# Optimization experiments

Measured on AMD Instinct MI355X. Metric: run time of the kernel, lower is better.

## Reference

```python
import jax, jax.numpy as jnp
import numpy as np

D = 128      # hidden_dim
NH = 4       # nhead
FF = 64      # dim_feedforward
P = 16       # patch size
C, H, W = 3, 224, 224
NA = 15      # n_actions
BS = 256
NP = (H // P) * (W // P)      # 196 patches
PD = C * P * P                # 768 patch_dim


def _ln(x, s, b):
    m = jnp.mean(x, -1, keepdims=True)
    v = jnp.mean(jnp.square(x - m), -1, keepdims=True)
    return (x - m) / jnp.sqrt(v + 1e-5) * s + b


def _mha(q, k, v, Wqkv, bqkv, Wo, bo):
    # q,k,v: (L, B, D); Wqkv: (D, 3D) jax-layout; torch MultiheadAttention math
    Wq, Wk, Wv = jnp.split(Wqkv, 3, axis=1)
    bq, bk, bv = jnp.split(bqkv, 3)
    hd = D // NH
    Lq, B, _ = q.shape
    Lk = k.shape[0]
    Q = (q @ Wq + bq).reshape(Lq, B, NH, hd)
    K = (k @ Wk + bk).reshape(Lk, B, NH, hd)
    V = (v @ Wv + bv).reshape(Lk, B, NH, hd)
    scores = jnp.einsum('qbhd,kbhd->bhqk', Q, K) * np.float32(1.0 / np.sqrt(hd))
    attn = jax.nn.softmax(scores, axis=-1)
    out = jnp.einsum('bhqk,kbhd->qbhd', attn, V).reshape(Lq, B, D)
    return out @ Wo + bo


def setup_inputs() -> dict:
    key = jax.random.key(0)
    ks = iter(jax.random.split(key, 64))
    n = lambda shape, sc=0.02: (jax.random.normal(next(ks), shape, jnp.float32) * sc)
    inp = {
        'image': jax.random.normal(next(ks), (BS, C, H, W), jnp.float32),
        'angle': jax.random.normal(next(ks), (BS,), jnp.float32),
        'pos_x': jax.random.normal(next(ks), (BS,), jnp.float32),
        'pos_y': jax.random.normal(next(ks), (BS,), jnp.float32),
        'sk': jax.random.normal(next(ks), (BS, 200), jnp.float32),
        'patch_W': n((PD, D)), 'patch_b': n((D,)),
        'pos_emb': n((NP, 1, D), 1.0),
        'enc_qkv_W': n((D, 3 * D)), 'enc_qkv_b': n((3 * D,)),
        'enc_out_W': n((D, D)), 'enc_out_b': n((D,)),
        'enc_ln1_s': jnp.ones((D,)), 'enc_ln1_b': jnp.zeros((D,)),
        'enc_ff1_W': n((D, FF)), 'enc_ff1_b': n((FF,)),
        'enc_ff2_W': n((FF, D)), 'enc_ff2_b': n((D,)),
        'enc_ln2_s': jnp.ones((D,)), 'enc_ln2_b': jnp.zeros((D,)),
        'dec_sa_qkv_W': n((D, 3 * D)), 'dec_sa_qkv_b': n((3 * D,)),
        'dec_sa_out_W': n((D, D)), 'dec_sa_out_b': n((D,)),
        'dec_ca_qkv_W': n((D, 3 * D)), 'dec_ca_qkv_b': n((3 * D,)),
        'dec_ca_out_W': n((D, D)), 'dec_ca_out_b': n((D,)),
        'dec_ln1_s': jnp.ones((D,)), 'dec_ln1_b': jnp.zeros((D,)),
        'dec_ln2_s': jnp.ones((D,)), 'dec_ln2_b': jnp.zeros((D,)),
        'dec_ln3_s': jnp.ones((D,)), 'dec_ln3_b': jnp.zeros((D,)),
        'dec_ff1_W': n((D, FF)), 'dec_ff1_b': n((FF,)),
        'dec_ff2_W': n((FF, D)), 'dec_ff2_b': n((D,)),
        'dec_norm_s': jnp.ones((D,)), 'dec_norm_b': jnp.zeros((D,)),
        'sk1_W': n((200, 256)), 'sk1_b': n((256,)),
        'sk2_W': n((256, 256)), 'sk2_b': n((256,)),
        'sk3_W': n((256, 100)), 'sk3_b': n((100,)),
        'act_W': n((NA + 103, D)), 'act_b': n((D,)),
        'l1_W': n((D, D)), 'l1_b': n((D,)),
        'l2_W': n((D, 1)), 'l2_b': n((1,)),
    }
    return inp


def reference(image, angle, pos_x, pos_y, sk,
              patch_W, patch_b, pos_emb,
              enc_qkv_W, enc_qkv_b, enc_out_W, enc_out_b,
              enc_ln1_s, enc_ln1_b, enc_ff1_W, enc_ff1_b, enc_ff2_W, enc_ff2_b,
              enc_ln2_s, enc_ln2_b,
              dec_sa_qkv_W, dec_sa_qkv_b, dec_sa_out_W, dec_sa_out_b,
              dec_ca_qkv_W, dec_ca_qkv_b, dec_ca_out_W, dec_ca_out_b,
              dec_ln1_s, dec_ln1_b, dec_ln2_s, dec_ln2_b, dec_ln3_s, dec_ln3_b,
              dec_ff1_W, dec_ff1_b, dec_ff2_W, dec_ff2_b,
              dec_norm_s, dec_norm_b,
              sk1_W, sk1_b, sk2_W, sk2_b, sk3_W, sk3_b,
              act_W, act_b, l1_W, l1_b, l2_W, l2_b):
    b = image.shape[0]
    hh, ww = H // P, W // P
    # rearrange 'b c (h p1) (w p2) -> b (h w) (p1 p2 c)'
    x = image.reshape(b, C, hh, P, ww, P).transpose(0, 2, 4, 3, 5, 1).reshape(b, hh * ww, PD)
    src = (x @ patch_W + patch_b).transpose(1, 0, 2) + pos_emb  # (n, b, D)
    # encoder layer (post-norm, dropout=eval)
    s2 = _mha(src, src, src, enc_qkv_W, enc_qkv_b, enc_out_W, enc_out_b)
    src = _ln(src + s2, enc_ln1_s, enc_ln1_b)
    ff = jax.nn.relu(src @ enc_ff1_W + enc_ff1_b) @ enc_ff2_W + enc_ff2_b
    memory = _ln(src + ff, enc_ln2_s, enc_ln2_b)
    # sketch MLP
    s = jax.nn.relu(sk @ sk1_W + sk1_b)
    s = jax.nn.relu(s @ sk2_W + sk2_b)
    s = s @ sk3_W + sk3_b  # (b, 100)
    pos_ang = jnp.stack([angle, pos_x, pos_y], axis=1)  # (b, 3)
    # batched action encoding (replaces python double loop)
    nA = NA
    eye = jnp.broadcast_to(jnp.eye(nA, dtype=image.dtype)[None], (b, nA, nA))
    feats = jnp.concatenate([
        eye,
        jnp.broadcast_to(pos_ang[:, None, :], (b, nA, 3)),
        jnp.broadcast_to(s[:, None, :], (b, nA, 100)),
    ], axis=-1)  # (b, nA, nA+103)
    tgt = (feats @ act_W + act_b).transpose(1, 0, 2)  # (nA, b, D)
    # decoder layer (post-norm)
    t2 = _mha(tgt, tgt, tgt, dec_sa_qkv_W, dec_sa_qkv_b, dec_sa_out_W, dec_sa_out_b)
    tgt = _ln(tgt + t2, dec_ln1_s, dec_ln1_b)
    t2 = _mha(tgt, memory, memory, dec_ca_qkv_W, dec_ca_qkv_b, dec_ca_out_W, dec_ca_out_b)
    tgt = _ln(tgt + t2, dec_ln2_s, dec_ln2_b)
    ff = jax.nn.relu(tgt @ dec_ff1_W + dec_ff1_b) @ dec_ff2_W + dec_ff2_b
    tgt = _ln(tgt + ff, dec_ln3_s, dec_ln3_b)
    out = _ln(tgt, dec_norm_s, dec_norm_b)  # (nA, b, D)
    out = out.transpose(1, 0, 2)  # (b, nA, D)
    q = jax.nn.relu(out @ l1_W + l1_b) @ l2_W + l2_b  # (b, nA, 1)
    return q[..., 0]  # (b, nA)
```

## Files before the change

### kernel.cpp

```cpp
#include <hip/hip_runtime.h>
#include <math.h>

#define BSZ 256
#define DIM 128
#define NHD 4
#define NPATCH 196
#define NACT 15

typedef float f32x4 __attribute__((ext_vector_type(4)));
typedef __bf16 bf16x8 __attribute__((ext_vector_type(8)));
typedef short short8 __attribute__((ext_vector_type(8)));

__device__ __forceinline__ float wred_sum(float v) {
#pragma unroll
    for (int m = 1; m < 64; m <<= 1) v += __shfl_xor(v, m, 64);
    return v;
}
__device__ __forceinline__ float wred_max(float v) {
#pragma unroll
    for (int m = 1; m < 64; m <<= 1) v = fmaxf(v, __shfl_xor(v, m, 64));
    return v;
}
__device__ __forceinline__ ushort f2bf(float f) {
    unsigned u = __float_as_uint(f);
    return (ushort)((u + 0x7fffu + ((u >> 16) & 1u)) >> 16);
}

__global__ __launch_bounds__(256) void k_wconv(
    const float* __restrict__ pW, const float* __restrict__ qkvW,
    const float* __restrict__ outW, const float* __restrict__ ff1W,
    const float* __restrict__ ff2W, const float* __restrict__ ckvW,
    ushort* __restrict__ o)
{
    int i = blockIdx.x * 256 + threadIdx.x;
    if (i < 98304) {
        int n = i / 768, kp = i % 768;
        int c = kp >> 8, q = kp & 255;
        o[i] = f2bf(pW[(q * 3 + c) * 128 + n]); return;
    }
    i -= 98304;
    if (i < 49152) { int n = i >> 7, k = i & 127; o[98304 + i] = f2bf(qkvW[k * 384 + n]); return; }
    i -= 49152;
    if (i < 16384) { int n = i >> 7, k = i & 127; o[147456 + i] = f2bf(outW[k * 128 + n]); return; }
    i -= 16384;
    if (i < 8192)  { int n = i >> 7, k = i & 127; o[163840 + i] = f2bf(ff1W[k * 64 + n]); return; }
    i -= 8192;
    if (i < 8192)  { int n = i >> 6, k = i & 63;  o[172032 + i] = f2bf(ff2W[k * 128 + n]); return; }
    i -= 8192;
    if (i < 32768) { int n = i >> 7, k = i & 127; o[180224 + i] = f2bf(ckvW[k * 384 + 128 + n]); return; }
}

__global__ __launch_bounds__(512) void k_pg_dec1(
    const float* __restrict__ img, const ushort* __restrict__ Wt,
    const float* __restrict__ pbias, const float* __restrict__ pe,
    float* __restrict__ C,
    const ushort* __restrict__ qkvWt, const float* __restrict__ qkvB,
    ushort* __restrict__ QKVb,
    const float* __restrict__ sk,
    const float* __restrict__ W1, const float* __restrict__ b1,
    const float* __restrict__ W2, const float* __restrict__ b2,
    const float* __restrict__ W3, const float* __restrict__ b3,
    const float* __restrict__ ang, const float* __restrict__ px,
    const float* __restrict__ py,
    const float* __restrict__ actW, const float* __restrict__ actb,
    const float* __restrict__ saW, const float* __restrict__ sab,
    const float* __restrict__ saoW, const float* __restrict__ saob,
    const float* __restrict__ ln1s, const float* __restrict__ ln1b,
    const float* __restrict__ caW, const float* __restrict__ cab,
    float* __restrict__ TGo, float* __restrict__ DQ)
{
    extern __shared__ char smem[];
    const int t = threadIdx.x;
    const int w = t >> 6, l = t & 63;

    if (blockIdx.x >= 256) {
        ushort* As = (ushort*)smem;
        ushort* Ws = As + 2 * 64 * 64;
        const bool act = t < 256;
        const int pb = blockIdx.x - 256;
        const int p = pb >> 2, bq = pb & 3;
        const int hp_ = p / 14, wp = p % 14;
        const int r0 = p * 256 + bq * 64;
        const int wm = w >> 1, wn = w & 1;
        const int lrow = l & 15, lk = l >> 4;
        const int arow = (t & 255) >> 2;
        const int b_img = bq * 64 + arow;
        const float* gimg = img + (size_t)b_img * 150528 + hp_ * 3584 + wp * 16;

        f32x4 acc[2][4];
#pragma unroll
        for (int m = 0; m < 2; ++m)
#pragma unroll
            for (int n = 0; n < 4; ++n) acc[m][n] = (f32x4)0.f;

        float4 va[4];
        short8 wr[4];

        auto loadT = [&](int kc) {
            if (!act) return;
            const int c = kc >> 8, p1q = (kc >> 6) & 3;
            const float* gc = gimg + c * 50176 + p1q * 896;
#pragma unroll
            for (int i = 0; i < 4; ++i)
                va[i] = *(const float4*)(gc + i * 224 + (t & 3) * 4);
#pragma unroll
            for (int j = 0; j < 4; ++j) {
                const int i2 = t + 256 * j;
                const int row = i2 >> 3, ch = i2 & 7;
                wr[j] = *(const short8*)(Wt + (size_t)row * 768 + kc + ch * 8);
            }
        };
        auto storeT = [&](int buf) {
            if (!act) return;
            ushort* Ab = As + buf * 64 * 64;
            ushort* Wb = Ws + buf * 128 * 64;
#pragma unroll
            for (int i = 0; i < 4; ++i) {
                ushort4 o4;
                o4.x = f2bf(va[i].x); o4.y = f2bf(va[i].y);
                o4.z = f2bf(va[i].z); o4.w = f2bf(va[i].w);
                const int kq = (t & 3) + 4 * i;
                const int bo = (kq * 8) ^ ((arow & 7) << 4);
                *(ushort4*)((char*)Ab + arow * 128 + bo) = o4;
            }
#pragma unroll
            for (int j = 0; j < 4; ++j) {
                const int i2 = t + 256 * j;
                const int row = i2 >> 3, ch = i2 & 7;
                const int sw = (ch * 16) ^ ((row & 7) << 4);
                *(short8*)((char*)Wb + row * 128 + sw) = wr[j];
            }
        };
        auto mfmaT = [&](int buf) {
            if (!act) return;
            const ushort* Ab = As + buf * 64 * 64;
            const ushort* Wb = Ws + buf * 128 * 64;
#pragma unroll
            for (int ks = 0; ks < 2; ++ks) {
                bf16x8 af[2], bfr[4];
#pragma unroll
                for (int m = 0; m < 2; ++m) {
                    const int row = wm * 32 + m * 16 + lrow;
                    const int col = (ks * 64 + lk * 16) ^ ((row & 7) << 4);
                    af[m] = *(const bf16x8*)((const char*)Ab + row * 128 + col);
                }
#pragma unroll
                for (int n = 0; n < 4; ++n) {
                    const int row = wn * 64 + n * 16 + lrow;
                    const int col = (ks * 64 + lk * 16) ^ ((row & 7) << 4);
                    bfr[n] = *(const bf16x8*)((const char*)Wb + row * 128 + col);
                }
#pragma unroll
                for (int m = 0; m < 2; ++m)
#pragma unroll
                    for (int n = 0; n < 4; ++n)
                        acc[m][n] = __builtin_amdgcn_mfma_f32_16x16x32_bf16(
                            af[m], bfr[n], acc[m][n], 0, 0, 0);
            }
        };

        loadT(0);
        for (int it = 0; it < 12; it += 2) {
            storeT(0);
            if (it + 1 < 12) loadT((it + 1) * 64);
            __syncthreads();
            mfmaT(0);
            storeT(1);
            if (it + 2 < 12) loadT((it + 2) * 64);
            __syncthreads();
            mfmaT(1);
        }

        __syncthreads();
        const int crow0 = (l >> 4) * 4;
        const int ccol = l & 15;
        if (act) {
#pragma unroll
            for (int m = 0; m < 2; ++m) {
                const int rowb = wm * 32 + m * 16 + crow0;
#pragma unroll
                for (int n = 0; n < 4; ++n) {
                    const int col = wn * 64 + n * 16 + ccol;
                    const float bv = pbias[col] + pe[p * 128 + col];
#pragma unroll
                    for (int j = 0; j < 4; ++j) {
                        const int row = rowb + j;
                        const float v = acc[m][n][j] + bv;
                        C[(size_t)(r0 + row) * 128 + col] = v;
                        const int bo = row * 256 + (((col >> 3) * 16) ^ ((row & 7) << 4)) + (col & 7) * 2;
                        *(ushort*)((char*)As + bo) = f2bf(v);
                    }
                }
            }
        }

        const int wm2 = w >> 1;
        const int wn2 = w & 1;
        for (int cc = 0; cc < 3; ++cc) {
            __syncthreads();
            for (int i = t; i < 2048; i += 512) {
                const int row = i >> 4, ch = i & 15;
                *(short8*)((char*)Ws + row * 256 + ((ch * 16) ^ ((row & 7) << 4))) =
                    *(const short8*)(qkvWt + (size_t)(cc * 128 + row) * 128 + ch * 8);
            }
            __syncthreads();
            f32x4 a2[4];
#pragma unroll
            for (int n = 0; n < 4; ++n) a2[n] = (f32x4)0.f;
#pragma unroll
            for (int ks = 0; ks < 4; ++ks) {
                const int arow2 = wm2 * 16 + lrow;
                const int acol = (ks * 64 + lk * 16) ^ ((arow2 & 7) << 4);
                const bf16x8 af = *(const bf16x8*)((const char*)As + arow2 * 256 + acol);
#pragma unroll
                for (int n = 0; n < 4; ++n) {
                    const int brow = wn2 * 64 + n * 16 + lrow;
                    const int bcol = (ks * 64 + lk * 16) ^ ((brow & 7) << 4);
                    const bf16x8 bf = *(const bf16x8*)((const char*)Ws + brow * 256 + bcol);
                    a2[n] = __builtin_amdgcn_mfma_f32_16x16x32_bf16(af, bf, a2[n], 0, 0, 0);
                }
            }
#pragma unroll
            for (int n = 0; n < 4; ++n) {
                const int gcol = cc * 128 + wn2 * 64 + n * 16 + ccol;
                const float bb = qkvB[gcol];
#pragma unroll
                for (int j = 0; j < 4; ++j) {
                    const int grow = r0 + wm2 * 16 + crow0 + j;
                    QKVb[(size_t)grow * 384 + gcol] = f2bf(a2[n][j] + bb);
                }
            }
        }
        return;
    }

    float* tg  = (float*)smem;
    float* qkv = tg + 1920;
    float* ao  = qkv + 5820;
    float* xr  = ao + 1920;
    float* h1  = xr + 256;
    float* h2  = h1 + 256;
    float* s3  = h2 + 256;
    float* pbv = s3 + 100;
    float* hp  = pbv + 64;
    const int b = blockIdx.x;

    {
        float pf = 0.f;
#define PFW(P, N) for (int i = t * 32; i < (N); i += 512 * 32) pf += P[i];
        PFW(W1, 200 * 256)
        PFW(W2, 256 * 256)
        PFW(W3, 256 * 100)
        PFW(actW, 118 * 128)
        PFW(saW, 128 * 384)
        PFW(saoW, 128 * 128)
        PFW(caW, 128 * 384)
#undef PFW
        asm volatile("" :: "v"(pf));
    }

    if (t < 256) xr[t] = (t < 200) ? sk[(size_t)b * 200 + t] : 0.f;
    __syncthreads();
    {
        const int c = t & 255, g = t >> 8;
        const int k0 = g * 100;
        float a = 0.f;
#pragma unroll 10
        for (int k = k0; k < k0 + 100; ++k) a += xr[k] * W1[k * 256 + c];
        hp[g * 256 + c] = a;
    }
    __syncthreads();
    if (t < 256) h1[t] = fmaxf(hp[t] + hp[256 + t] + b1[t], 0.f);
    __syncthreads();
    {
        const int c = t & 255, g = t >> 8;
        const int k0 = g * 128;
        float a = 0.f;
#pragma unroll 8
        for (int k = k0; k < k0 + 128; ++k) a += h1[k] * W2[k * 256 + c];
        hp[g * 256 + c] = a;
    }
    __syncthreads();
    if (t < 256) h2[t] = fmaxf(hp[t] + hp[256 + t] + b2[t], 0.f);
    __syncthreads();
    if (t < 400) {
        const int c = t % 100, g = t / 100;
        const int k0 = g * 64;
        float a = 0.f;
#pragma unroll 8
        for (int k = k0; k < k0 + 64; ++k) a += h2[k] * W3[k * 100 + c];
        hp[g * 256 + c] = a;
    }
    __syncthreads();
    if (t < 100) s3[t] = hp[t] + hp[256 + t] + hp[512 + t] + hp[768 + t] + b3[t];
    __syncthreads();
    {
        const int c = t & 127, g = t >> 7;
        const int k0 = g * 25;
        float a = 0.f;
#pragma unroll 5
        for (int k = k0; k < k0 + 25; ++k) a += s3[k] * actW[(18 + k) * 128 + c];
        hp[g * 256 + c] = a;
    }
    __syncthreads();
    if (t < 128) {
        const float base = actb[t] + hp[t] + hp[256 + t] + hp[512 + t] + hp[768 + t] +
                           ang[b] * actW[15 * 128 + t] + px[b] * actW[16 * 128 + t] +
                           py[b] * actW[17 * 128 + t];
#pragma unroll
        for (int i = 0; i < 15; ++i) tg[i * 128 + t] = base + actW[i * 128 + t];
    }
    __syncthreads();

    if (t < 384) {
        float acc[15];
#pragma unroll
        for (int r = 0; r < 15; ++r) acc[r] = 0.f;
#pragma unroll 4
        for (int k = 0; k < 128; ++k) {
            const float wv = saW[(size_t)k * 384 + t];
#pragma unroll
            for (int r = 0; r < 15; ++r) acc[r] += tg[r * 128 + k] * wv;
        }
        const float bb = sab[t];
#pragma unroll
        for (int r = 0; r < 15; ++r) qkv[r * 388 + t] = acc[r] + bb;
    }
    __syncthreads();

    const float rs = 0.17677669529663687f;
    if (w < 4) {
        for (int qi = 0; qi < 15; ++qi) {
            float s = -3.0e38f;
            if (l < 15) {
                s = 0.f;
#pragma unroll
                for (int d = 0; d < 32; ++d)
                    s += qkv[qi * 388 + w * 32 + d] * qkv[l * 388 + 128 + w * 32 + d];
                s *= rs;
            }
            const float m = wred_max(s);
            const float pv = (l < 15) ? __expf(s - m) : 0.f;
            const float sum = wred_sum(pv);
            if (l < 15) pbv[w * 16 + l] = pv;
            if (l < 32) {
                float o = 0.f;
#pragma unroll
                for (int j = 0; j < 15; ++j) o += pbv[w * 16 + j] * qkv[j * 388 + 256 + w * 32 + l];
                ao[qi * 128 + w * 32 + l] = o / sum;
            }
        }
    }
    __syncthreads();

    {
        const int c = t & 127, g = t >> 7;
        const int r3 = (g + 12 < 15) ? g + 12 : 0;
        float a0 = 0.f, a1 = 0.f, a2 = 0.f, a3 = 0.f;
#pragma unroll 4
        for (int k = 0; k < 128; ++k) {
            const float wv = saoW[(size_t)k * 128 + c];
            a0 += ao[g * 128 + k] * wv;
            a1 += ao[(g + 4) * 128 + k] * wv;
            a2 += ao[(g + 8) * 128 + k] * wv;
            a3 += ao[r3 * 128 + k] * wv;
        }
        const float bb = saob[c];
        qkv[g * 388 + c]       = a0 + bb + tg[g * 128 + c];
        qkv[(g + 4) * 388 + c] = a1 + bb + tg[(g + 4) * 128 + c];
        qkv[(g + 8) * 388 + c] = a2 + bb + tg[(g + 8) * 128 + c];
        if (g + 12 < 15) qkv[(g + 12) * 388 + c] = a3 + bb + tg[(g + 12) * 128 + c];
    }
    __syncthreads();
    for (int r = w; r < 15; r += 8) {
        const float x0 = qkv[r * 388 + l], x1 = qkv[r * 388 + l + 64];
        const float sm = wred_sum(x0 + x1);
        const float sq = wred_sum(x0 * x0 + x1 * x1);
        const float mean = sm * 0.0078125f;
        const float rstd = rsqrtf(sq * 0.0078125f - mean * mean + 1e-5f);
        const float y0 = (x0 - mean) * rstd * ln1s[l] + ln1b[l];
        const float y1 = (x1 - mean) * rstd * ln1s[l + 64] + ln1b[l + 64];
        tg[r * 128 + l] = y0; tg[r * 128 + l + 64] = y1;
        float* g2 = TGo + ((size_t)r * 256 + b) * 128;
        g2[l] = y0; g2[l + 64] = y1;
    }
    __syncthreads();

    {
        const int c = t & 127, g = t >> 7;
        const int r3 = (g + 12 < 15) ? g + 12 : 0;
        float a0 = 0.f, a1 = 0.f, a2 = 0.f, a3 = 0.f;
#pragma unroll 4
        for (int k = 0; k < 128; ++k) {
            const float wv = caW[(size_t)k * 384 + c];
            a0 += tg[g * 128 + k] * wv;
            a1 += tg[(g + 4) * 128 + k] * wv;
            a2 += tg[(g + 8) * 128 + k] * wv;
            a3 += tg[r3 * 128 + k] * wv;
        }
        const float bb = cab[c];
        DQ[((size_t)g * 256 + b) * 128 + c]       = a0 + bb;
        DQ[((size_t)(g + 4) * 256 + b) * 128 + c] = a1 + bb;
        DQ[((size_t)(g + 8) * 256 + b) * 128 + c] = a2 + bb;
        if (g + 12 < 15) DQ[((size_t)(g + 12) * 256 + b) * 128 + c] = a3 + bb;
    }
}

template <int FF, int CKV>
__global__ __launch_bounds__(256) void k_gemm_ln(
    const ushort* __restrict__ A, int lda,
    const ushort* __restrict__ Wt, int K,
    const float* __restrict__ bias,
    const float* __restrict__ resid,
    const float* __restrict__ lns, const float* __restrict__ lnbi,
    float* __restrict__ Co, ushort* __restrict__ Cb,
    const ushort* __restrict__ ffW, const float* __restrict__ ffb,
    ushort* __restrict__ Fb,
    const ushort* __restrict__ ckvW, const float* __restrict__ ckvB,
    float* __restrict__ KVout)
{
    __shared__ ushort As[64 * 64];
    __shared__ ushort Ws[128 * 64];
    __shared__ float psum[64][2][2];
    __shared__ ushort ffWs[FF ? 64 * 128 : 2];
    __shared__ ushort ckvWs[CKV ? 64 * 128 : 2];
    const int t = threadIdx.x;
    const int w = t >> 6, l = t & 63;
    const int r0 = blockIdx.x * 64;
    const int wm = w >> 1, wn = w & 1;
    const int lrow = l & 15, lk = l >> 4;

    f32x4 acc[2][4];
#pragma unroll
    for (int m = 0; m < 2; ++m)
#pragma unroll
        for (int n = 0; n < 4; ++n) acc[m][n] = (f32x4)0.f;

    for (int kc = 0; kc < K; kc += 64) {
        __syncthreads();
#pragma unroll
        for (int i = t; i < 64 * 8; i += 256) {
            const int row = i >> 3, ch = i & 7;
            const int sw = (ch * 16) ^ ((row & 7) << 4);
            *(short8*)((char*)As + row * 128 + sw) =
                *(const short8*)(A + (size_t)(r0 + row) * lda + kc + ch * 8);
        }
#pragma unroll
        for (int i = t; i < 128 * 8; i += 256) {
            const int row = i >> 3, ch = i & 7;
            const int sw = (ch * 16) ^ ((row & 7) << 4);
            *(short8*)((char*)Ws + row * 128 + sw) =
                *(const short8*)(Wt + (size_t)row * K + kc + ch * 8);
        }
        __syncthreads();
#pragma unroll
        for (int ks = 0; ks < 2; ++ks) {
            bf16x8 af[2], bfr[4];
#pragma unroll
            for (int m = 0; m < 2; ++m) {
                const int row = wm * 32 + m * 16 + lrow;
                const int col = (ks * 64 + lk * 16) ^ ((row & 7) << 4);
                af[m] = *(const bf16x8*)((const char*)As + row * 128 + col);
            }
#pragma unroll
            for (int n = 0; n < 4; ++n) {
                const int row = wn * 64 + n * 16 + lrow;
                const int col = (ks * 64 + lk * 16) ^ ((row & 7) << 4);
                bfr[n] = *(const bf16x8*)((const char*)Ws + row * 128 + col);
            }
#pragma unroll
            for (int m = 0; m < 2; ++m)
#pragma unroll
                for (int n = 0; n < 4; ++n)
                    acc[m][n] = __builtin_amdgcn_mfma_f32_16x16x32_bf16(
                        af[m], bfr[n], acc[m][n], 0, 0, 0);
        }
    }

    const int crow0 = (l >> 4) * 4;
    const int ccol = l & 15;
#pragma unroll
    for (int m = 0; m < 2; ++m) {
        const int growb = r0 + wm * 32 + m * 16 + crow0;
#pragma unroll
        for (int n = 0; n < 4; ++n) {
            const int gcol = wn * 64 + n * 16 + ccol;
            const float bv = bias[gcol];
#pragma unroll
            for (int j = 0; j < 4; ++j) {
                float v = acc[m][n][j] + bv;
                if (resid) v += resid[(size_t)(growb + j) * 128 + gcol];
                acc[m][n][j] = v;
            }
        }
    }
#pragma unroll
    for (int m = 0; m < 2; ++m)
#pragma unroll
        for (int j = 0; j < 4; ++j) {
            float s_ = 0.f, q_ = 0.f;
#pragma unroll
            for (int n = 0; n < 4; ++n) {
                const float x = acc[m][n][j];
                s_ += x; q_ += x * x;
            }
#pragma unroll
            for (int mk = 1; mk < 16; mk <<= 1) {
                s_ += __shfl_xor(s_, mk, 64);
                q_ += __shfl_xor(q_, mk, 64);
            }
            if (ccol == 0) {
                const int r = wm * 32 + m * 16 + crow0 + j;
                psum[r][wn][0] = s_;
                psum[r][wn][1] = q_;
            }
        }
    __syncthreads();
    float mean_[2][4], rstd_[2][4];
#pragma unroll
    for (int m = 0; m < 2; ++m)
#pragma unroll
        for (int j = 0; j < 4; ++j) {
            const int r = wm * 32 + m * 16 + crow0 + j;
            const float sum = psum[r][0][0] + psum[r][1][0];
            const float sq  = psum[r][0][1] + psum[r][1][1];
            const float mean = sum * 0.0078125f;
            const float var = sq * 0.0078125f - mean * mean;
            mean_[m][j] = mean;
            rstd_[m][j] = rsqrtf(var + 1e-5f);
        }
#pragma unroll
    for (int m = 0; m < 2; ++m) {
        const int growb = r0 + wm * 32 + m * 16 + crow0;
#pragma unroll
        for (int n = 0; n < 4; ++n) {
            const int gcol = wn * 64 + n * 16 + ccol;
            const float sv = lns[gcol], bv2 = lnbi[gcol];
#pragma unroll
            for (int j = 0; j < 4; ++j) {
                const float y = (acc[m][n][j] - mean_[m][j]) * rstd_[m][j] * sv + bv2;
                acc[m][n][j] = y;
                const size_t oi = (size_t)(growb + j) * 128 + gcol;
                if (Co) Co[oi] = y;
                if (Cb) Cb[oi] = f2bf(y);
            }
        }
    }

    if constexpr (FF || CKV) {
#pragma unroll
        for (int m = 0; m < 2; ++m) {
            const int rowb = wm * 32 + m * 16 + crow0;
#pragma unroll
            for (int n = 0; n < 4; ++n) {
                const int c = wn * 64 + n * 16 + ccol;
                const int cb = ((c >> 3) * 16);
#pragma unroll
                for (int j = 0; j < 4; ++j) {
                    const int row = rowb + j;
                    const int bo = row * 256 + ((cb) ^ ((row & 7) << 4)) + (c & 7) * 2;
                    *(ushort*)((char*)Ws + bo) = f2bf(acc[m][n][j]);
                }
            }
        }
    }

    if constexpr (FF) {
        for (int i = t; i < 1024; i += 256) {
            const int row = i >> 4, ch = i & 15;
            *(short8*)((char*)ffWs + row * 256 + ((ch * 16) ^ ((row & 7) << 4))) =
                *(const short8*)(ffW + (size_t)row * 128 + ch * 8);
        }
        __syncthreads();
        f32x4 accF[4];
#pragma unroll
        for (int n = 0; n < 4; ++n) accF[n] = (f32x4)0.f;
#pragma unroll
        for (int ks = 0; ks < 4; ++ks) {
            const int arow2 = w * 16 + lrow;
            const int acol = (ks * 64 + lk * 16) ^ ((arow2 & 7) << 4);
            const bf16x8 af = *(const bf16x8*)((const char*)Ws + arow2 * 256 + acol);
#pragma unroll
            for (int n = 0; n < 4; ++n) {
                const int brow = n * 16 + lrow;
                const int bcol = (ks * 64 + lk * 16) ^ ((brow & 7) << 4);
                const bf16x8 bf = *(const bf16x8*)((const char*)ffWs + brow * 256 + bcol);
                accF[n] = __builtin_amdgcn_mfma_f32_16x16x32_bf16(af, bf, accF[n], 0, 0, 0);
            }
        }
#pragma unroll
        for (int n = 0; n < 4; ++n) {
            const int gcol = n * 16 + ccol;
            const float bb = ffb[gcol];
#pragma unroll
            for (int j = 0; j < 4; ++j) {
                const int grow = r0 + w * 16 + crow0 + j;
                Fb[(size_t)grow * 64 + gcol] = f2bf(fmaxf(accF[n][j] + bb, 0.f));
            }
        }
    }

    if constexpr (CKV) {
        for (int cc = 0; cc < 4; ++cc) {
            __syncthreads();
            for (int i = t; i < 1024; i += 256) {
                const int row = i >> 4, ch = i & 15;
                *(short8*)((char*)ckvWs + row * 256 + ((ch * 16) ^ ((row & 7) << 4))) =
                    *(const short8*)(ckvW + (size_t)(cc * 64 + row) * 128 + ch * 8);
            }
            __syncthreads();
            f32x4 accC[4];
#pragma unroll
            for (int n = 0; n < 4; ++n) accC[n] = (f32x4)0.f;
#pragma unroll
            for (int ks = 0; ks < 4; ++ks) {
                const int arow2 = w * 16 + lrow;
                const int acol = (ks * 64 + lk * 16) ^ ((arow2 & 7) << 4);
                const bf16x8 af = *(const bf16x8*)((const char*)Ws + arow2 * 256 + acol);
#pragma unroll
                for (int n = 0; n < 4; ++n) {
                    const int brow = n * 16 + lrow;
                    const int bcol = (ks * 64 + lk * 16) ^ ((brow & 7) << 4);
                    const bf16x8 bf = *(const bf16x8*)((const char*)ckvWs + brow * 256 + bcol);
                    accC[n] = __builtin_amdgcn_mfma_f32_16x16x32_bf16(af, bf, accC[n], 0, 0, 0);
                }
            }
#pragma unroll
            for (int n = 0; n < 4; ++n) {
                const int gcol = cc * 64 + n * 16 + ccol;
                const float bb = ckvB[gcol];
#pragma unroll
                for (int j = 0; j < 4; ++j) {
                    const int grow = r0 + w * 16 + crow0 + j;
                    KVout[(size_t)grow * 256 + gcol] = accC[n][j] + bb;
                }
            }
        }
    }
}

__global__ __launch_bounds__(256) void k_attn_mfma(
    const ushort* __restrict__ qkv, ushort* __restrict__ ob, float scale)
{
    __shared__ ushort Ks[208 * 40];
    __shared__ ushort Vt[32 * 232];
    __shared__ ushort Ps[4][16 * 232];
    const int bh = blockIdx.x;
    const int b = bh >> 2, h = bh & 3;
    const int t = threadIdx.x, w = t >> 6, l = t & 63;
    const int lr = l & 15, lg = l >> 4;

    for (int idx = t; idx < 784; idx += 256) {
        const int j = idx >> 2, ch = idx & 3;
        const size_t base = ((size_t)j * 256 + b) * 384 + h * 32 + ch * 8;
        *(short8*)(Ks + j * 40 + ch * 8) = *(const short8*)(qkv + base + 128);
        short8 v = *(const short8*)(qkv + base + 256);
#pragma unroll
        for (int q = 0; q < 8; ++q)
            Vt[(ch * 8 + q) * 232 + j] = (ushort)v[q];
    }
    for (int idx = t; idx < 32 * 36; idx += 256)
        Vt[(idx / 36) * 232 + 196 + (idx % 36)] = 0;
    for (int i = l; i < 256; i += 64)
        Ps[w][(i >> 4) * 232 + 208 + (i & 15)] = 0;
    __syncthreads();

    for (int qt = w; qt < 13; qt += 4) {
        int qr = qt * 16 + lr; if (qr > 195) qr = 195;
        const bf16x8 qf = *(const bf16x8*)(qkv + ((size_t)qr * 256 + b) * 384 + h * 32 + lg * 8);

        f32x4 s[13];
#pragma unroll
        for (int jn = 0; jn < 13; ++jn) {
            const bf16x8 kf = *(const bf16x8*)(Ks + (jn * 16 + lr) * 40 + lg * 8);
            s[jn] = __builtin_amdgcn_mfma_f32_16x16x32_bf16(qf, kf, (f32x4)0.f, 0, 0, 0);
        }
        if (lr >= 4) {
            s[12][0] = -3.0e38f; s[12][1] = -3.0e38f;
            s[12][2] = -3.0e38f; s[12][3] = -3.0e38f;
        }

        float inv[4];
        ushort* pw = Ps[w];
#pragma unroll
        for (int j = 0; j < 4; ++j) {
            float m = s[0][j];
#pragma unroll
            for (int jn = 1; jn < 13; ++jn) m = fmaxf(m, s[jn][j]);
            m = fmaxf(m, __shfl_xor(m, 1, 64));
            m = fmaxf(m, __shfl_xor(m, 2, 64));
            m = fmaxf(m, __shfl_xor(m, 4, 64));
            m = fmaxf(m, __shfl_xor(m, 8, 64));
            float sum = 0.f;
#pragma unroll
            for (int jn = 0; jn < 13; ++jn) {
                const float p = __expf((s[jn][j] - m) * scale);
                s[jn][j] = p;
                sum += p;
            }
            sum += __shfl_xor(sum, 1, 64);
            sum += __shfl_xor(sum, 2, 64);
            sum += __shfl_xor(sum, 4, 64);
            sum += __shfl_xor(sum, 8, 64);
            inv[j] = 1.0f / sum;
        }
#pragma unroll
        for (int jn = 0; jn < 13; ++jn)
#pragma unroll
            for (int j = 0; j < 4; ++j)
                pw[(lg * 4 + j) * 232 + jn * 16 + lr] = f2bf(s[jn][j]);

        f32x4 o0 = (f32x4)0.f, o1 = (f32x4)0.f;
#pragma unroll
        for (int kt = 0; kt < 7; ++kt) {
            const bf16x8 pf = *(const bf16x8*)(pw + lr * 232 + kt * 32 + lg * 8);
            const bf16x8 v0 = *(const bf16x8*)(Vt + lr * 232 + kt * 32 + lg * 8);
            const bf16x8 v1 = *(const bf16x8*)(Vt + (16 + lr) * 232 + kt * 32 + lg * 8);
            o0 = __builtin_amdgcn_mfma_f32_16x16x32_bf16(pf, v0, o0, 0, 0, 0);
            o1 = __builtin_amdgcn_mfma_f32_16x16x32_bf16(pf, v1, o1, 0, 0, 0);
        }
#pragma unroll
        for (int j = 0; j < 4; ++j) {
            const int r = qt * 16 + lg * 4 + j;
            if (r < 196) {
                const size_t o = ((size_t)r * 256 + b) * 128 + h * 32;
                ob[o + lr]      = f2bf(o0[j] * inv[j]);
                ob[o + 16 + lr] = f2bf(o1[j] * inv[j]);
            }
        }
    }
}

__global__ __launch_bounds__(256) void k_attn(
    const float* __restrict__ qp, int qstride,
    const float* __restrict__ kvp, int kvstride, int koff, int voff,
    float* __restrict__ op, ushort* __restrict__ ob,
    int Lq, int Lk, float scale)
{
    __shared__ float Kl[196 * 36];
    __shared__ float Vl[196 * 32];
    __shared__ float pbuf[4][256];
    const int bh = blockIdx.x;
    const int b = bh >> 2;
    const int h = bh & 3;
    const int t = threadIdx.x;
    const int w = t >> 6;
    const int l = t & 63;

    for (int idx = t; idx < Lk * 8; idx += 256) {
        const int j = idx >> 3;
        const int kq = idx & 7;
        const size_t row = ((size_t)j * 256 + b) * kvstride + h * 32 + kq * 4;
        *(float4*)(&Kl[j * 36 + kq * 4]) = *(const float4*)(kvp + row + koff);
        *(float4*)(&Vl[j * 32 + kq * 4]) = *(const float4*)(kvp + row + voff);
    }
    if ((Lk & 1) && t < 8) *(float4*)(&Vl[Lk * 32 + t * 4]) = make_float4(0.f, 0.f, 0.f, 0.f);
    __syncthreads();

    const int Lh = (Lk + 1) >> 1;
    const int half = l >> 5;
    const int kk = l & 31;
    const int jb = half * Lh;

    for (int jq = w; jq < Lq; jq += 4) {
        const float* qrow = qp + ((size_t)jq * 256 + b) * qstride + h * 32;
        float4 q4[8];
#pragma unroll
        for (int kq = 0; kq < 8; ++kq) q4[kq] = *(const float4*)(qrow + kq * 4);

        float s[4];
#pragma unroll
        for (int r = 0; r < 4; ++r) {
            const int j = l + (r << 6);
            float acc = -3.0e38f;
            if (j < Lk) {
                acc = 0.f;
#pragma unroll
                for (int kq = 0; kq < 8; ++kq) {
                    const float4 kv = *(const float4*)(&Kl[j * 36 + kq * 4]);
                    acc += q4[kq].x * kv.x + q4[kq].y * kv.y +
                           q4[kq].z * kv.z + q4[kq].w * kv.w;
                }
                acc *= scale;
            }
            s[r] = acc;
        }
        float m = fmaxf(fmaxf(s[0], s[1]), fmaxf(s[2], s[3]));
        m = wred_max(m);
        float sum = 0.f;
#pragma unroll
        for (int r = 0; r < 4; ++r) {
            const int j = l + (r << 6);
            float p = __expf(s[r] - m);
            if (j >= Lk) p = 0.f;
            pbuf[w][j] = p;
            sum += p;
        }
        sum = wred_sum(sum);
        const float inv = 1.0f / sum;
        __threadfence_block();

        float o = 0.f;
        for (int jj = 0; jj < Lh; ++jj) {
            const float pv = pbuf[w][jb + jj];
            const float vv = Vl[(jb + jj) * 32 + kk];
            o += pv * vv;
        }
        o += __shfl_xor(o, 32, 64);
        o *= inv;
        if (l < 32) {
            const size_t oi = ((size_t)jq * 256 + b) * 128 + h * 32 + l;
            if (op) op[oi] = o;
            if (ob) ob[oi] = f2bf(o);
        }
        __threadfence_block();
    }
}

__global__ __launch_bounds__(512) void k_dec2(
    const float* __restrict__ TGo, const float* __restrict__ AT,
    const float* __restrict__ caoW, const float* __restrict__ caob,
    const float* __restrict__ ln2s, const float* __restrict__ ln2b,
    const float* __restrict__ ff1W, const float* __restrict__ ff1b,
    const float* __restrict__ ff2W, const float* __restrict__ ff2b,
    const float* __restrict__ ln3s, const float* __restrict__ ln3b,
    const float* __restrict__ ns, const float* __restrict__ nb,
    const float* __restrict__ l1W, const float* __restrict__ l1b,
    const float* __restrict__ l2w, const float* __restrict__ l2b,
    float* __restrict__ qout)
{
    __shared__ float tg[15][128], ao[15][128], o2[15][128];
    __shared__ float ff[15][64];
    const int b = blockIdx.x, t = threadIdx.x;
    const int w = t >> 6, l = t & 63;

    {
        float pf = 0.f;
#define PFW(P, N) for (int i = t * 32; i < (N); i += 512 * 32) pf += P[i];
        PFW(caoW, 128 * 128)
        PFW(ff1W, 128 * 64)
        PFW(ff2W, 64 * 128)
        PFW(l1W, 128 * 128)
#undef PFW
        asm volatile("" :: "v"(pf));
    }

    for (int idx = t; idx < 1920; idx += 512) {
        const int r = idx >> 7, c = idx & 127;
        tg[r][c] = TGo[((size_t)r * 256 + b) * 128 + c];
        ao[r][c] = AT[((size_t)r * 256 + b) * 128 + c];
    }
    __syncthreads();

    {
        const int c = t & 127, g = t >> 7;
        const int r3 = (g + 12 < 15) ? g + 12 : 0;
        float a0 = 0.f, a1 = 0.f, a2 = 0.f, a3 = 0.f;
#pragma unroll 4
        for (int k = 0; k < 128; ++k) {
            const float wv = caoW[(size_t)k * 128 + c];
            a0 += ao[g][k] * wv;
            a1 += ao[g + 4][k] * wv;
            a2 += ao[g + 8][k] * wv;
            a3 += ao[r3][k] * wv;
        }
        const float bb = caob[c];
        o2[g][c]     = a0 + bb + tg[g][c];
        o2[g + 4][c] = a1 + bb + tg[g + 4][c];
        o2[g + 8][c] = a2 + bb + tg[g + 8][c];
        if (g + 12 < 15) o2[g + 12][c] = a3 + bb + tg[g + 12][c];
    }
    __syncthreads();
    for (int r = w; r < 15; r += 8) {
        const float x0 = o2[r][l], x1 = o2[r][l + 64];
        const float sm = wred_sum(x0 + x1);
        const float sq = wred_sum(x0 * x0 + x1 * x1);
        const float mean = sm * 0.0078125f;
        const float rstd = rsqrtf(sq * 0.0078125f - mean * mean + 1e-5f);
        tg[r][l]      = (x0 - mean) * rstd * ln2s[l] + ln2b[l];
        tg[r][l + 64] = (x1 - mean) * rstd * ln2s[l + 64] + ln2b[l + 64];
    }
    __syncthreads();
    {
        const int n = t & 63, g = t >> 6;
        const int r1 = (g + 8 < 15) ? g + 8 : 0;
        float a0 = 0.f, a1 = 0.f;
#pragma unroll 4
        for (int k = 0; k < 128; ++k) {
            const float wv = ff1W[(size_t)k * 64 + n];
            a0 += tg[g][k] * wv;
            a1 += tg[r1][k] * wv;
        }
        const float bb = ff1b[n];
        ff[g][n] = fmaxf(a0 + bb, 0.f);
        if (g + 8 < 15) ff[g + 8][n] = fmaxf(a1 + bb, 0.f);
    }
    __syncthreads();
    {
        const int c = t & 127, g = t >> 7;
        const int r3 = (g + 12 < 15) ? g + 12 : 0;
        float a0 = 0.f, a1 = 0.f, a2 = 0.f, a3 = 0.f;
#pragma unroll 4
        for (int k = 0; k < 64; ++k) {
            const float wv = ff2W[(size_t)k * 128 + c];
            a0 += ff[g][k] * wv;
            a1 += ff[g + 4][k] * wv;
            a2 += ff[g + 8][k] * wv;
            a3 += ff[r3][k] * wv;
        }
        const float bb = ff2b[c];
        o2[g][c]     = a0 + bb + tg[g][c];
        o2[g + 4][c] = a1 + bb + tg[g + 4][c];
        o2[g + 8][c] = a2 + bb + tg[g + 8][c];
        if (g + 12 < 15) o2[g + 12][c] = a3 + bb + tg[g + 12][c];
    }
    __syncthreads();
    for (int r = w; r < 15; r += 8) {
        const float x0 = o2[r][l], x1 = o2[r][l + 64];
        const float sm = wred_sum(x0 + x1);
        const float sq = wred_sum(x0 * x0 + x1 * x1);
        const float mean = sm * 0.0078125f;
        const float rstd = rsqrtf(sq * 0.0078125f - mean * mean + 1e-5f);
        const float y0 = (x0 - mean) * rstd * ln3s[l] + ln3b[l];
        const float y1 = (x1 - mean) * rstd * ln3s[l + 64] + ln3b[l + 64];
        const float sm2 = wred_sum(y0 + y1);
        const float sq2 = wred_sum(y0 * y0 + y1 * y1);
        const float mean2 = sm2 * 0.0078125f;
        const float rstd2 = rsqrtf(sq2 * 0.0078125f - mean2 * mean2 + 1e-5f);
        tg[r][l]      = (y0 - mean2) * rstd2 * ns[l] + nb[l];
        tg[r][l + 64] = (y1 - mean2) * rstd2 * ns[l + 64] + nb[l + 64];
    }
    __syncthreads();
    {
        const int c = t & 127, g = t >> 7;
        const int r3 = (g + 12 < 15) ? g + 12 : 0;
        float a0 = 0.f, a1 = 0.f, a2 = 0.f, a3 = 0.f;
#pragma unroll 4
        for (int k = 0; k < 128; ++k) {
            const float wv = l1W[(size_t)k * 128 + c];
            a0 += tg[g][k] * wv;
            a1 += tg[g + 4][k] * wv;
            a2 += tg[g + 8][k] * wv;
            a3 += tg[r3][k] * wv;
        }
        const float bb = l1b[c];
        o2[g][c]     = fmaxf(a0 + bb, 0.f);
        o2[g + 4][c] = fmaxf(a1 + bb, 0.f);
        o2[g + 8][c] = fmaxf(a2 + bb, 0.f);
        if (g + 12 < 15) o2[g + 12][c] = fmaxf(a3 + bb, 0.f);
    }
    __syncthreads();
    for (int r = w; r < 15; r += 8) {
        const float d = wred_sum(o2[r][l] * l2w[l] + o2[r][l + 64] * l2w[l + 64]);
        if (l == 0) qout[b * 15 + r] = d + l2b[0];
    }
}

extern "C" void kernel_launch(void* const* d_in, const int* in_sizes, int n_in,
                              void* d_out, int out_size, void* d_ws, size_t ws_size,
                              hipStream_t stream)
{
    (void)in_sizes; (void)n_in; (void)out_size; (void)ws_size;
    const float* image      = (const float*)d_in[0];
    const float* angle      = (const float*)d_in[1];
    const float* pos_x      = (const float*)d_in[2];
    const float* pos_y      = (const float*)d_in[3];
    const float* sk         = (const float*)d_in[4];
    const float* patch_W    = (const float*)d_in[5];
    const float* patch_b    = (const float*)d_in[6];
    const float* pos_emb    = (const float*)d_in[7];
    const float* enc_qkv_W  = (const float*)d_in[8];
    const float* enc_qkv_b  = (const float*)d_in[9];
    const float* enc_out_W  = (const float*)d_in[10];
    const float* enc_out_b  = (const float*)d_in[11];
    const float* enc_ln1_s  = (const float*)d_in[12];
    const float* enc_ln1_b  = (const float*)d_in[13];
    const float* enc_ff1_W  = (const float*)d_in[14];
    const float* enc_ff1_b  = (const float*)d_in[15];
    const float* enc_ff2_W  = (const float*)d_in[16];
    const float* enc_ff2_b  = (const float*)d_in[17];
    const float* enc_ln2_s  = (const float*)d_in[18];
    const float* enc_ln2_b  = (const float*)d_in[19];
    const float* dec_sa_qkv_W = (const float*)d_in[20];
    const float* dec_sa_qkv_b = (const float*)d_in[21];
    const float* dec_sa_out_W = (const float*)d_in[22];
    const float* dec_sa_out_b = (const float*)d_in[23];
    const float* dec_ca_qkv_W = (const float*)d_in[24];
    const float* dec_ca_qkv_b = (const float*)d_in[25];
    const float* dec_ca_out_W = (const float*)d_in[26];
    const float* dec_ca_out_b = (const float*)d_in[27];
    const float* dec_ln1_s  = (const float*)d_in[28];
    const float* dec_ln1_b  = (const float*)d_in[29];
    const float* dec_ln2_s  = (const float*)d_in[30];
    const float* dec_ln2_b  = (const float*)d_in[31];
    const float* dec_ln3_s  = (const float*)d_in[32];
    const float* dec_ln3_b  = (const float*)d_in[33];
    const float* dec_ff1_W  = (const float*)d_in[34];
    const float* dec_ff1_b  = (const float*)d_in[35];
    const float* dec_ff2_W  = (const float*)d_in[36];
    const float* dec_ff2_b  = (const float*)d_in[37];
    const float* dec_norm_s = (const float*)d_in[38];
    const float* dec_norm_b = (const float*)d_in[39];
    const float* sk1_W = (const float*)d_in[40];
    const float* sk1_b = (const float*)d_in[41];
    const float* sk2_W = (const float*)d_in[42];
    const float* sk2_b = (const float*)d_in[43];
    const float* sk3_W = (const float*)d_in[44];
    const float* sk3_b = (const float*)d_in[45];
    const float* act_W = (const float*)d_in[46];
    const float* act_b = (const float*)d_in[47];
    const float* l1_W  = (const float*)d_in[48];
    const float* l1_b  = (const float*)d_in[49];
    const float* l2_W  = (const float*)d_in[50];
    const float* l2_b  = (const float*)d_in[51];

    float* ws = (float*)d_ws;
    float* S0   = ws;
    float* QKVr = ws + 6422528;
    float* T0   = ws + 25690112;
    float* T1   = ws + 32112640;
    float* F1   = ws + 38535168;
    float* M0r  = ws + 41746432;
    float* S1s  = ws + 48168960;
    float* TG   = S1s + 156672;
    ushort* WTS = (ushort*)(ws + 48817152);

    ushort* QKVb = (ushort*)QKVr;
    float*  KV   = QKVr;
    float* DQ   = QKVr + 14319616;
    float* DT0  = T0;
    ushort* T0b  = (ushort*)M0r;
    ushort* F1b  = (ushort*)F1;
    ushort* wt_patch = WTS;
    ushort* wt_qkv   = WTS + 98304;
    ushort* wt_out   = WTS + 147456;
    ushort* wt_ff1   = WTS + 163840;
    ushort* wt_ff2   = WTS + 172032;
    ushort* wt_ckv   = WTS + 180224;
    (void)T1;

    const float rs = 0.17677669529663687f;

    k_wconv<<<dim3(832), 256, 0, stream>>>(patch_W, enc_qkv_W, enc_out_W,
                                           enc_ff1_W, enc_ff2_W, dec_ca_qkv_W, WTS);

    k_pg_dec1<<<dim3(1040), 512, 49152, stream>>>(
        image, wt_patch, patch_b, pos_emb, S0,
        wt_qkv, enc_qkv_b, QKVb,
        sk, sk1_W, sk1_b, sk2_W, sk2_b, sk3_W, sk3_b,
        angle, pos_x, pos_y, act_W, act_b,
        dec_sa_qkv_W, dec_sa_qkv_b, dec_sa_out_W, dec_sa_out_b,
        dec_ln1_s, dec_ln1_b, dec_ca_qkv_W, dec_ca_qkv_b, TG, DQ);

    k_attn_mfma<<<dim3(1024), 256, 0, stream>>>(QKVb, T0b, rs);
    k_gemm_ln<1, 0><<<dim3(784), 256, 0, stream>>>(
        T0b, 128, wt_out, 128, enc_out_b, S0, enc_ln1_s, enc_ln1_b, S0, nullptr,
        wt_ff1, enc_ff1_b, F1b, nullptr, nullptr, nullptr);
    k_gemm_ln<0, 1><<<dim3(784), 256, 0, stream>>>(
        F1b, 64, wt_ff2, 64, enc_ff2_b, S0, enc_ln2_s, enc_ln2_b, nullptr, nullptr,
        nullptr, nullptr, nullptr, wt_ckv, dec_ca_qkv_b + 128, KV);

    k_attn<<<dim3(1024), 256, 0, stream>>>(DQ, 128, KV, 256, 0, 128,
                                           DT0, nullptr, 15, 196, rs);
    k_dec2<<<dim3(256), 512, 0, stream>>>(
        TG, DT0, dec_ca_out_W, dec_ca_out_b, dec_ln2_s, dec_ln2_b,
        dec_ff1_W, dec_ff1_b, dec_ff2_W, dec_ff2_b,
        dec_ln3_s, dec_ln3_b, dec_norm_s, dec_norm_b,
        l1_W, l1_b, l2_W, l2_b, (float*)d_out);
}
```

Baseline: 280.7 us.

## Shrink fused patch/decoder kernel LDS to raise occupancy

The patch-embedding GEMM drops from double-buffered to single-buffered LDS tiles and adds a barrier each k-step. The QKV projection now stages the weight in 64-row chunks over six passes instead of 128-row chunks over three. The decoder branch overlays its scratch buffers onto the qkv region. Together these cut dynamic shared memory from 48KB to 40KB so more blocks can be resident per CU, at the cost of extra synchronisation and less load/compute overlap.

```diff
diff --git a/kernel.cpp b/kernel.cpp
--- a/kernel.cpp
+++ b/kernel.cpp
@@ -75,7 +75,8 @@
 
     if (blockIdx.x >= 256) {
         ushort* As = (ushort*)smem;
-        ushort* Ws = As + 2 * 64 * 64;
+        ushort* WsP = As + 64 * 64;
+        ushort* Wq = As + 8192;
         const bool act = t < 256;
         const int pb = blockIdx.x - 256;
         const int p = pb >> 2, bq = pb & 3;
@@ -110,10 +111,8 @@
                 wr[j] = *(const short8*)(Wt + (size_t)row * 768 + kc + ch * 8);
             }
         };
-        auto storeT = [&](int buf) {
+        auto storeT = [&]() {
             if (!act) return;
-            ushort* Ab = As + buf * 64 * 64;
-            ushort* Wb = Ws + buf * 128 * 64;
 #pragma unroll
             for (int i = 0; i < 4; ++i) {
                 ushort4 o4;
@@ -121,20 +120,18 @@
                 o4.z = f2bf(va[i].z); o4.w = f2bf(va[i].w);
                 const int kq = (t & 3) + 4 * i;
                 const int bo = (kq * 8) ^ ((arow & 7) << 4);
-                *(ushort4*)((char*)Ab + arow * 128 + bo) = o4;
+                *(ushort4*)((char*)As + arow * 128 + bo) = o4;
             }
 #pragma unroll
             for (int j = 0; j < 4; ++j) {
                 const int i2 = t + 256 * j;
                 const int row = i2 >> 3, ch = i2 & 7;
                 const int sw = (ch * 16) ^ ((row & 7) << 4);
-                *(short8*)((char*)Wb + row * 128 + sw) = wr[j];
+                *(short8*)((char*)WsP + row * 128 + sw) = wr[j];
             }
         };
-        auto mfmaT = [&](int buf) {
+        auto mfmaT = [&]() {
             if (!act) return;
-            const ushort* Ab = As + buf * 64 * 64;
-            const ushort* Wb = Ws + buf * 128 * 64;
 #pragma unroll
             for (int ks = 0; ks < 2; ++ks) {
                 bf16x8 af[2], bfr[4];
@@ -142,13 +139,13 @@
                 for (int m = 0; m < 2; ++m) {
                     const int row = wm * 32 + m * 16 + lrow;
                     const int col = (ks * 64 + lk * 16) ^ ((row & 7) << 4);
-                    af[m] = *(const bf16x8*)((const char*)Ab + row * 128 + col);
+                    af[m] = *(const bf16x8*)((const char*)As + row * 128 + col);
                 }
 #pragma unroll
                 for (int n = 0; n < 4; ++n) {
                     const int row = wn * 64 + n * 16 + lrow;
                     const int col = (ks * 64 + lk * 16) ^ ((row & 7) << 4);
-                    bfr[n] = *(const bf16x8*)((const char*)Wb + row * 128 + col);
+                    bfr[n] = *(const bf16x8*)((const char*)WsP + row * 128 + col);
                 }
 #pragma unroll
                 for (int m = 0; m < 2; ++m)
@@ -160,15 +157,12 @@
         };
 
         loadT(0);
-        for (int it = 0; it < 12; it += 2) {
-            storeT(0);
+        for (int it = 0; it < 12; ++it) {
+            __syncthreads();
+            storeT();
             if (it + 1 < 12) loadT((it + 1) * 64);
             __syncthreads();
-            mfmaT(0);
-            storeT(1);
-            if (it + 2 < 12) loadT((it + 2) * 64);
-            __syncthreads();
-            mfmaT(1);
+            mfmaT();
         }
 
         __syncthreads();
@@ -196,33 +190,33 @@
 
         const int wm2 = w >> 1;
         const int wn2 = w & 1;
-        for (int cc = 0; cc < 3; ++cc) {
+        for (int cc = 0; cc < 6; ++cc) {
+            if (cc) __syncthreads();
+            for (int i = t; i < 1024; i += 512) {
+                const int row = i >> 4, ch = i & 15;
+                *(short8*)((char*)Wq + row * 256 + ((ch * 16) ^ ((row & 7) << 4))) =
+                    *(const short8*)(qkvWt + (size_t)(cc * 64 + row) * 128 + ch * 8);
+            }
             __syncthreads();
-            for (int i = t; i < 2048; i += 512) {
-                const int row = i >> 4, ch = i & 15;
-                *(short8*)((char*)Ws + row * 256 + ((ch * 16) ^ ((row & 7) << 4))) =
-                    *(const short8*)(qkvWt + (size_t)(cc * 128 + row) * 128 + ch * 8);
-            }
-            __syncthreads();
-            f32x4 a2[4];
-#pragma unroll
-            for (int n = 0; n < 4; ++n) a2[n] = (f32x4)0.f;
+            f32x4 a2[2];
+#pragma unroll
+            for (int n = 0; n < 2; ++n) a2[n] = (f32x4)0.f;
 #pragma unroll
             for (int ks = 0; ks < 4; ++ks) {
                 const int arow2 = wm2 * 16 + lrow;
                 const int acol = (ks * 64 + lk * 16) ^ ((arow2 & 7) << 4);
                 const bf16x8 af = *(const bf16x8*)((const char*)As + arow2 * 256 + acol);
 #pragma unroll
-                for (int n = 0; n < 4; ++n) {
-                    const int brow = wn2 * 64 + n * 16 + lrow;
+                for (int n = 0; n < 2; ++n) {
+                    const int brow = wn2 * 32 + n * 16 + lrow;
                     const int bcol = (ks * 64 + lk * 16) ^ ((brow & 7) << 4);
-                    const bf16x8 bf = *(const bf16x8*)((const char*)Ws + brow * 256 + bcol);
+                    const bf16x8 bf = *(const bf16x8*)((const char*)Wq + brow * 256 + bcol);
                     a2[n] = __builtin_amdgcn_mfma_f32_16x16x32_bf16(af, bf, a2[n], 0, 0, 0);
                 }
             }
 #pragma unroll
-            for (int n = 0; n < 4; ++n) {
-                const int gcol = cc * 128 + wn2 * 64 + n * 16 + ccol;
+            for (int n = 0; n < 2; ++n) {
+                const int gcol = cc * 64 + wn2 * 32 + n * 16 + ccol;
                 const float bb = qkvB[gcol];
 #pragma unroll
                 for (int j = 0; j < 4; ++j) {
@@ -237,12 +231,12 @@
     float* tg  = (float*)smem;
     float* qkv = tg + 1920;
     float* ao  = qkv + 5820;
-    float* xr  = ao + 1920;
-    float* h1  = xr + 256;
-    float* h2  = h1 + 256;
-    float* s3  = h2 + 256;
-    float* pbv = s3 + 100;
-    float* hp  = pbv + 64;
+    float* pbv = ao + 1920;
+    float* xr  = qkv;
+    float* h1  = qkv + 256;
+    float* h2  = qkv + 512;
+    float* s3  = qkv + 768;
+    float* hp  = qkv + 868;
     const int b = blockIdx.x;
 
     {
@@ -1044,7 +1038,7 @@
     k_wconv<<<dim3(832), 256, 0, stream>>>(patch_W, enc_qkv_W, enc_out_W,
                                            enc_ff1_W, enc_ff2_W, dec_ca_qkv_W, WTS);
 
-    k_pg_dec1<<<dim3(1040), 512, 49152, stream>>>(
+    k_pg_dec1<<<dim3(1040), 512, 40960, stream>>>(
         image, wt_patch, patch_b, pos_emb, S0,
         wt_qkv, enc_qkv_b, QKVb,
         sk, sk1_W, sk1_b, sk2_W, sk2_b, sk3_W, sk3_b,
```

Result: no change. 282.5 us (+0.7%).
